# Optimization experiments

Hardware: AMD Instinct MI355X
Metric: run time of the kernel (lower is better)

Reference implementation:

```python
import jax, jax.numpy as jnp
import numpy as np

B, S, D, H = 4, 2048, 1024, 16
DEPTH = D // H


def setup_inputs() -> dict:
    key = jax.random.key(0)
    ks = jax.random.split(key, 12)
    inp = {
        "Q": jax.random.normal(ks[0], (B, S, D), jnp.float32),
        "K": jax.random.normal(ks[1], (B, S, D), jnp.float32),
        "V": jax.random.normal(ks[2], (B, S, D), jnp.float32),
        "mask": jax.random.randint(ks[3], (B, 1, S, S), 0, 2, jnp.int32),
        "Wq": jax.random.normal(ks[4], (D, D), jnp.float32) / np.sqrt(D),
        "bq": jnp.zeros((D,), jnp.float32),
        "Wk": jax.random.normal(ks[5], (D, D), jnp.float32) / np.sqrt(D),
        "bk": jnp.zeros((D,), jnp.float32),
        "Wv": jax.random.normal(ks[6], (D, D), jnp.float32) / np.sqrt(D),
        "bv": jnp.zeros((D,), jnp.float32),
        "Wo": jax.random.normal(ks[7], (D, D), jnp.float32) / np.sqrt(D),
        "bo": jnp.zeros((D,), jnp.float32),
    }
    return inp


def _split_heads(x):
    # (B, S, D) -> (B, H, S, depth)
    b, s, _ = x.shape
    return x.reshape(b, s, H, DEPTH).transpose(0, 2, 1, 3)


def reference(Q, K, V, mask, Wq, bq, Wk, bk, Wv, bv, Wo, bo):
    q = _split_heads(Q @ Wq + bq)  # (B,H,S,d)
    k = _split_heads(K @ Wk + bk)
    v = _split_heads(V @ Wv + bv)
    scores = jnp.einsum("bhqd,bhkd->bhqk", q, k) / jnp.sqrt(jnp.float32(DEPTH))
    m = mask.astype(jnp.bool_).astype(jnp.float32)  # (B,1,S,S)
    scores = scores + (1.0 - m) * -1e9
    attn = jax.nn.softmax(scores, axis=-1)  # (B,H,S,S)
    ctx = jnp.einsum("bhqk,bhkd->bhqd", attn, v)
    ctx = ctx.transpose(0, 2, 1, 3).reshape(Q.shape[0], -1, D)  # (B,S,D)
    out = ctx @ Wo + bo
    return out, attn
```

## Files before the change

kernel.cpp:

```cpp
#include <hip/hip_runtime.h>
#include <hip/hip_bf16.h>

#define B_ 4
#define S_ 2048
#define D_ 1024
#define H_ 16
#define TSZ 8388608L

typedef short short8 __attribute__((ext_vector_type(8)));
typedef float f32x4 __attribute__((ext_vector_type(4)));

__device__ inline unsigned short f2b(float f) {
  __hip_bfloat16 h = __float2bfloat16(f);
  return __builtin_bit_cast(unsigned short, h);
}
__device__ inline void gld16(const unsigned short* g, unsigned short* l) {
  __builtin_amdgcn_global_load_lds(
      (const __attribute__((address_space(1))) void*)g,
      (__attribute__((address_space(3))) void*)l, 16, 0, 0);
}

__global__ __launch_bounds__(256) void mask_pack(const int* __restrict__ mask,
                                                 unsigned int* __restrict__ mp) {
  long t = (long)blockIdx.x * 256 + threadIdx.x;
  const int4* p = (const int4*)(mask + (t >> 4) * (long)S_ + (t & 15) * 128);
  unsigned int w0 = 0, w1 = 0, w2 = 0, w3 = 0;
#pragma unroll
  for (int c = 0; c < 32; c++) {
    int4 v = p[c];
#pragma unroll
    for (int e = 0; e < 4; e++) {
      int k = c * 4 + e;
      int val = e == 0 ? v.x : e == 1 ? v.y : e == 2 ? v.z : v.w;
      int nb = k >> 4, p16 = k & 15;
      int gg = p16 >> 2, r = p16 & 3;
      unsigned bit = ((unsigned)val & 1u) << (nb * 4 + r);
      if (gg == 0) w0 |= bit; else if (gg == 1) w1 |= bit;
      else if (gg == 2) w2 |= bit; else w3 |= bit;
    }
  }
  *(uint4*)(mp + t * 4) = make_uint4(w0, w1, w2, w3);
}

__global__ __launch_bounds__(256) void cvt3(
    const float* __restrict__ Q, const float* __restrict__ K,
    const float* __restrict__ V, unsigned short* __restrict__ qo,
    unsigned short* __restrict__ ko, unsigned short* __restrict__ vo) {
  int seg = blockIdx.x >> 12;
  long i = ((long)(blockIdx.x & 4095) * 256 + threadIdx.x) * 8;
  const float* in = seg == 0 ? Q : seg == 1 ? K : V;
  unsigned short* out = seg == 0 ? qo : seg == 1 ? ko : vo;
  float4 a = *(const float4*)(in + i);
  float4 b = *(const float4*)(in + i + 4);
  short8 u;
  u[0] = (short)f2b(a.x); u[1] = (short)f2b(a.y);
  u[2] = (short)f2b(a.z); u[3] = (short)f2b(a.w);
  u[4] = (short)f2b(b.x); u[5] = (short)f2b(b.y);
  u[6] = (short)f2b(b.z); u[7] = (short)f2b(b.w);
  *(short8*)(out + i) = u;
}

__global__ __launch_bounds__(256) void transpose_w(
    const float* __restrict__ W, unsigned short* __restrict__ Wt) {
  __shared__ unsigned short t[64 * 72];
  const int tid = threadIdx.x;
  const int k0 = blockIdx.x * 64, n0 = blockIdx.y * 64;
#pragma unroll
  for (int p = 0; p < 4; p++) {
    int e = (p * 256 + tid) * 4;
    int r = e >> 6, c = e & 63;
    float4 v = *(const float4*)(W + (long)(k0 + r) * D_ + n0 + c);
    ushort4 u;
    u.x = f2b(v.x); u.y = f2b(v.y); u.z = f2b(v.z); u.w = f2b(v.w);
    *(ushort4*)(&t[r * 72 + c]) = u;
  }
  __syncthreads();
#pragma unroll
  for (int p = 0; p < 2; p++) {
    int e = (p * 256 + tid) * 8;
    int n = e >> 6, kc = e & 63;
    short8 x;
#pragma unroll
    for (int i = 0; i < 8; i++) x[i] = (short)t[(kc + i) * 72 + n];
    *(short8*)(Wt + (long)(n0 + n) * D_ + k0 + kc) = x;
  }
}

template <int MODE>
__global__ __launch_bounds__(256) void gemm_kernel(
    const unsigned short* __restrict__ A, const unsigned short* __restrict__ Wt,
    const float* __restrict__ bias, void* __restrict__ outv,
    int M, int N, int K) {
  __shared__ unsigned short Asm[128 * 32];
  __shared__ unsigned short Bsm[128 * 32];
  const int tid = threadIdx.x;
  const int lane = tid & 63, wid = tid >> 6;
  const int g = lane >> 4, li = lane & 15;
  const int wm = wid >> 1, wn = wid & 1;
  const long bm = (long)blockIdx.x * 128;
  const long bn = (long)blockIdx.y * 128;

  f32x4 acc[4][4];
#pragma unroll
  for (int i = 0; i < 4; i++)
#pragma unroll
    for (int j = 0; j < 4; j++) acc[i][j] = (f32x4){0.f, 0.f, 0.f, 0.f};

  for (int kt = 0; kt < K / 32; ++kt) {
    const int k0 = kt * 32;
    __syncthreads();
#pragma unroll
    for (int p = 0; p < 2; p++) {
      int ci = p * 256 + wid * 64 + lane;
      int r = ci >> 2, c = (ci & 3) * 8;
      gld16(A + (bm + r) * (long)K + k0 + c, &Asm[(p * 256 + wid * 64) * 8]);
      gld16(Wt + (bn + r) * (long)K + k0 + c, &Bsm[(p * 256 + wid * 64) * 8]);
    }
    __syncthreads();
    short8 af[4], bf[4];
#pragma unroll
    for (int i = 0; i < 4; i++)
      af[i] = *(const short8*)(&Asm[(wm * 64 + i * 16 + li) * 32 + g * 8]);
#pragma unroll
    for (int i = 0; i < 4; i++)
      bf[i] = *(const short8*)(&Bsm[(wn * 64 + i * 16 + li) * 32 + g * 8]);
#pragma unroll
    for (int i = 0; i < 4; i++)
#pragma unroll
      for (int j = 0; j < 4; j++)
        acc[i][j] =
            __builtin_amdgcn_mfma_f32_16x16x32_bf16(af[i], bf[j], acc[i][j], 0, 0, 0);
  }

#pragma unroll
  for (int i = 0; i < 4; i++) {
    int row0 = (int)bm + wm * 64 + i * 16 + g * 4;
#pragma unroll
    for (int j = 0; j < 4; j++) {
      int col = (int)bn + wn * 64 + j * 16 + li;
      float bvv = bias[col];
      if (MODE == 2) {
        int b = row0 >> 11, s0 = row0 & 2047;
        int h = col >> 6, dd = col & 63;
        ushort4 u;
#pragma unroll
        for (int jj = 0; jj < 4; jj++) u[jj] = f2b(acc[i][j][jj] + bvv);
        *(ushort4*)((unsigned short*)outv +
                    ((long)(b * H_ + h) * 64 + dd) * S_ + s0) = u;
      } else {
#pragma unroll
        for (int jj = 0; jj < 4; jj++) {
          int row = row0 + jj;
          float v = acc[i][j][jj] + bvv;
          if (MODE == 0) {
            ((float*)outv)[(long)row * N + col] = v;
          } else {
            int b = row >> 11, s = row & 2047;
            int h = col >> 6, dd = col & 63;
            ((unsigned short*)outv)[(((long)(b * H_ + h)) * S_ + s) * 64 + dd] =
                f2b(v);
          }
        }
      }
    }
  }
}

__global__ __launch_bounds__(256, 4) void attn_kernel(
    const unsigned short* __restrict__ q,
    const unsigned short* __restrict__ k,
    const unsigned short* __restrict__ vt,
    const unsigned int* __restrict__ mpk,
    float* __restrict__ attn,
    unsigned short* __restrict__ ctx) {
  __shared__ unsigned short k_lds[128 * 72];
  __shared__ unsigned short vt_lds[64 * 136];
  const int tid = threadIdx.x;
  const int lane = tid & 63, wid = tid >> 6;
  const int g = lane >> 4, li = lane & 15;
  const int bh = blockIdx.y;
  const int b = bh >> 4, h = bh & 15;
  const int qw = blockIdx.x * 64 + wid * 16;
  const int qs = qw + li;

  const unsigned short* qp = q + ((long)bh * S_ + qw) * 64;
  const short8 aq0 = *(const short8*)(qp + li * 64 + g * 8);
  const short8 aq1 = *(const short8*)(qp + li * 64 + 32 + g * 8);
  const unsigned int* mp = mpk + (((long)b * S_ + qs) * 16) * 4 + g;

  const unsigned short* kbase = k + (long)bh * S_ * 64;
  const unsigned short* vbase = vt + (long)bh * 64 * S_;
  int kst[4], kgo[4], vst[4], vgo[4];
#pragma unroll
  for (int p = 0; p < 4; p++) {
    int e = (p * 256 + tid) * 8;
    int krr = e >> 6, kcc = e & 63;
    kst[p] = krr * 72 + kcc;
    kgo[p] = krr * 64 + kcc;
    int vrr = e >> 7, vcc = e & 127;
    int c0 = ((vcc >> 5) << 5) + ((vcc & 8) << 1) + ((vcc & 16) >> 2);
    vst[p] = vrr * 136 + c0;
    vgo[p] = vrr * S_ + vcc;
  }

  float lsum = 0.f;
  short8 kreg[4];
#pragma unroll
  for (int p = 0; p < 4; p++)
    kreg[p] = *(const short8*)(kbase + kgo[p]);
  unsigned int mb_n = mp[0];
  for (int kt = 0; kt < 16; ++kt) {
    __syncthreads();
#pragma unroll
    for (int p = 0; p < 4; p++)
      *(short8*)(&k_lds[kst[p]]) = kreg[p];
    unsigned int mb = mb_n;
    if (kt < 15) {
#pragma unroll
      for (int p = 0; p < 4; p++)
        kreg[p] = *(const short8*)(kbase + (kt + 1) * 8192 + kgo[p]);
      mb_n = mp[(kt + 1) * 4];
    }
    __syncthreads();
#pragma unroll
    for (int nb = 0; nb < 8; nb++) {
      short8 b0 = *(const short8*)(&k_lds[(nb * 16 + li) * 72 + g * 8]);
      short8 b1 = *(const short8*)(&k_lds[(nb * 16 + li) * 72 + 32 + g * 8]);
      f32x4 s = (f32x4){0.f, 0.f, 0.f, 0.f};
      __builtin_amdgcn_s_setprio(1);
      s = __builtin_amdgcn_mfma_f32_16x16x32_bf16(b0, aq0, s, 0, 0, 0);
      s = __builtin_amdgcn_mfma_f32_16x16x32_bf16(b1, aq1, s, 0, 0, 0);
      __builtin_amdgcn_s_setprio(0);
#pragma unroll
      for (int r = 0; r < 4; r++) {
        float sc = s[r] * 0.125f + (((mb >> (nb * 4 + r)) & 1u) ? 0.f : -1e9f);
        lsum += __expf(sc);
      }
    }
  }
  lsum += __shfl_xor(lsum, 16);
  lsum += __shfl_xor(lsum, 32);
  const float linv = (lsum > 0.f) ? 1.0f / lsum : 0.f;

  f32x4 c[4];
#pragma unroll
  for (int i = 0; i < 4; i++) c[i] = (f32x4){0.f, 0.f, 0.f, 0.f};

  short8 vreg[4];
#pragma unroll
  for (int p = 0; p < 4; p++) {
    kreg[p] = *(const short8*)(kbase + kgo[p]);
    vreg[p] = *(const short8*)(vbase + vgo[p]);
  }
  mb_n = mp[0];
  for (int kt = 0; kt < 16; ++kt) {
    __syncthreads();
#pragma unroll
    for (int p = 0; p < 4; p++) {
      *(short8*)(&k_lds[kst[p]]) = kreg[p];
      ushort4* vh = (ushort4*)&vreg[p];
      *(ushort4*)(&vt_lds[vst[p]]) = vh[0];
      *(ushort4*)(&vt_lds[vst[p] + 8]) = vh[1];
    }
    unsigned int mb = mb_n;
    if (kt < 15) {
#pragma unroll
      for (int p = 0; p < 4; p++) {
        kreg[p] = *(const short8*)(kbase + (kt + 1) * 8192 + kgo[p]);
        vreg[p] = *(const short8*)(vbase + (kt + 1) * 128 + vgo[p]);
      }
      mb_n = mp[(kt + 1) * 4];
    }
    __syncthreads();
    float* arow = attn + ((long)bh * S_ + qs) * S_ + kt * 128;
    short8 pu2[4];
#pragma unroll
    for (int nb = 0; nb < 8; nb++) {
      short8 b0 = *(const short8*)(&k_lds[(nb * 16 + li) * 72 + g * 8]);
      short8 b1 = *(const short8*)(&k_lds[(nb * 16 + li) * 72 + 32 + g * 8]);
      f32x4 s = (f32x4){0.f, 0.f, 0.f, 0.f};
      __builtin_amdgcn_s_setprio(1);
      s = __builtin_amdgcn_mfma_f32_16x16x32_bf16(b0, aq0, s, 0, 0, 0);
      s = __builtin_amdgcn_mfma_f32_16x16x32_bf16(b1, aq1, s, 0, 0, 0);
      __builtin_amdgcn_s_setprio(0);
      f32x4 pf;
      ushort4 pu;
#pragma unroll
      for (int r = 0; r < 4; r++) {
        float sc = s[r] * 0.125f + (((mb >> (nb * 4 + r)) & 1u) ? 0.f : -1e9f);
        float pv = __expf(sc) * linv;
        pf[r] = pv;
        pu[r] = f2b(pv);
      }
      __builtin_nontemporal_store(pf, (f32x4*)(arow + nb * 16 + g * 4));
      ((ushort4*)&pu2[nb >> 1])[nb & 1] = pu;
    }
    __builtin_amdgcn_s_setprio(1);
#pragma unroll
    for (int kc = 0; kc < 4; kc++) {
      short8 ap = pu2[kc];
#pragma unroll
      for (int nb2 = 0; nb2 < 4; nb2++) {
        short8 bv =
            *(const short8*)(&vt_lds[(nb2 * 16 + li) * 136 + kc * 32 + g * 8]);
        c[nb2] = __builtin_amdgcn_mfma_f32_16x16x32_bf16(ap, bv, c[nb2], 0, 0, 0);
      }
    }
    __builtin_amdgcn_s_setprio(0);
  }

#pragma unroll
  for (int nb2 = 0; nb2 < 4; nb2++) {
#pragma unroll
    for (int j = 0; j < 4; j++) {
      int qrow = qw + g * 4 + j;
      ctx[((long)(b * S_ + qrow)) * D_ + h * 64 + nb2 * 16 + li] = f2b(c[nb2][j]);
    }
  }
}

extern "C" void kernel_launch(void* const* d_in, const int* in_sizes, int n_in,
                              void* d_out, int out_size, void* d_ws, size_t ws_size,
                              hipStream_t stream) {
  const float* Q = (const float*)d_in[0];
  const float* K = (const float*)d_in[1];
  const float* V = (const float*)d_in[2];
  const int* mask = (const int*)d_in[3];
  const float* Wq = (const float*)d_in[4];
  const float* bq = (const float*)d_in[5];
  const float* Wk = (const float*)d_in[6];
  const float* bk = (const float*)d_in[7];
  const float* Wv = (const float*)d_in[8];
  const float* bv = (const float*)d_in[9];
  const float* Wo = (const float*)d_in[10];
  const float* bo = (const float*)d_in[11];

  float* out = (float*)d_out;
  float* attn = out + TSZ;
  unsigned int* mpack = (unsigned int*)d_out;

  unsigned short* ws = (unsigned short*)d_ws;
  unsigned short* qh = ws;
  unsigned short* kh = ws + TSZ;
  unsigned short* vt = ws + 2 * TSZ;
  unsigned short* ctx = ws + 3 * TSZ;
  unsigned short* qbf = ws + 4 * TSZ;
  unsigned short* kbf = ws + 5 * TSZ;
  unsigned short* vbf = ws + 6 * TSZ;
  unsigned short* wtq = ws + 7 * TSZ;
  unsigned short* wtk = wtq + 1048576;
  unsigned short* wtv = wtk + 1048576;
  unsigned short* wto = wtv + 1048576;

  dim3 bb(256);
  mask_pack<<<512, bb, 0, stream>>>(mask, mpack);
  cvt3<<<12288, bb, 0, stream>>>(Q, K, V, qbf, kbf, vbf);
  transpose_w<<<dim3(16, 16), bb, 0, stream>>>(Wq, wtq);
  transpose_w<<<dim3(16, 16), bb, 0, stream>>>(Wk, wtk);
  transpose_w<<<dim3(16, 16), bb, 0, stream>>>(Wv, wtv);
  transpose_w<<<dim3(16, 16), bb, 0, stream>>>(Wo, wto);

  dim3 gg(64, 8);
  gemm_kernel<1><<<gg, bb, 0, stream>>>(qbf, wtq, bq, qh, 8192, 1024, 1024);
  gemm_kernel<1><<<gg, bb, 0, stream>>>(kbf, wtk, bk, kh, 8192, 1024, 1024);
  gemm_kernel<2><<<gg, bb, 0, stream>>>(vbf, wtv, bv, vt, 8192, 1024, 1024);
  attn_kernel<<<dim3(32, 64), bb, 0, stream>>>(qh, kh, vt, mpack, attn, ctx);
  gemm_kernel<0><<<gg, bb, 0, stream>>>(ctx, wto, bo, out, 8192, 1024, 1024);
}
```

Baseline: 559.7 us.

## Batch weight transposes and QKV GEMMs, read K directly from global in attention

Merges the four weight-transpose launches into one grid over z, and the three QKV projection GEMMs into one launch indexed by blockIdx.z. The Wo GEMM is specialised with constant sizes. In the attention kernel, K fragments are now loaded straight from global memory into registers, with no staging through LDS, which removes that LDS buffer and the barriers in the first pass. Blocks are also remapped so that each XCD handles a contiguous set of heads, for better L2 locality. The trade-off is more global or L2 traffic for K, with possible extra latency and less coalesced fragment loads, in exchange for less LDS use, fewer syncs and fewer launches.

```diff
diff --git a/kernel.cpp b/kernel.cpp
--- a/kernel.cpp
+++ b/kernel.cpp
@@ -60,9 +60,15 @@
   *(short8*)(out + i) = u;
 }
 
-__global__ __launch_bounds__(256) void transpose_w(
-    const float* __restrict__ W, unsigned short* __restrict__ Wt) {
+__global__ __launch_bounds__(256) void transpose_w4(
+    const float* __restrict__ W0, const float* __restrict__ W1,
+    const float* __restrict__ W2, const float* __restrict__ W3,
+    unsigned short* __restrict__ T0, unsigned short* __restrict__ T1,
+    unsigned short* __restrict__ T2, unsigned short* __restrict__ T3) {
   __shared__ unsigned short t[64 * 72];
+  const int z = blockIdx.z;
+  const float* W = z == 0 ? W0 : z == 1 ? W1 : z == 2 ? W2 : W3;
+  unsigned short* Wt = z == 0 ? T0 : z == 1 ? T1 : z == 2 ? T2 : T3;
   const int tid = threadIdx.x;
   const int k0 = blockIdx.x * 64, n0 = blockIdx.y * 64;
 #pragma unroll
@@ -86,11 +92,90 @@
   }
 }
 
-template <int MODE>
-__global__ __launch_bounds__(256) void gemm_kernel(
+__global__ __launch_bounds__(256) void qkv_gemm(
+    const unsigned short* __restrict__ qa, const unsigned short* __restrict__ ka,
+    const unsigned short* __restrict__ va, const unsigned short* __restrict__ wq,
+    const unsigned short* __restrict__ wk, const unsigned short* __restrict__ wv,
+    const float* __restrict__ bqp, const float* __restrict__ bkp,
+    const float* __restrict__ bvp, unsigned short* __restrict__ qo,
+    unsigned short* __restrict__ ko, unsigned short* __restrict__ vo) {
+  __shared__ unsigned short Asm[128 * 32];
+  __shared__ unsigned short Bsm[128 * 32];
+  const int z = blockIdx.z;
+  const unsigned short* A = z == 0 ? qa : z == 1 ? ka : va;
+  const unsigned short* Wt = z == 0 ? wq : z == 1 ? wk : wv;
+  const float* bias = z == 0 ? bqp : z == 1 ? bkp : bvp;
+  unsigned short* outp = z == 0 ? qo : z == 1 ? ko : vo;
+  const int tid = threadIdx.x;
+  const int lane = tid & 63, wid = tid >> 6;
+  const int g = lane >> 4, li = lane & 15;
+  const int wm = wid >> 1, wn = wid & 1;
+  const long bm = (long)blockIdx.x * 128;
+  const long bn = (long)blockIdx.y * 128;
+
+  f32x4 acc[4][4];
+#pragma unroll
+  for (int i = 0; i < 4; i++)
+#pragma unroll
+    for (int j = 0; j < 4; j++) acc[i][j] = (f32x4){0.f, 0.f, 0.f, 0.f};
+
+  for (int kt = 0; kt < 32; ++kt) {
+    const int k0 = kt * 32;
+    __syncthreads();
+#pragma unroll
+    for (int p = 0; p < 2; p++) {
+      int ci = p * 256 + wid * 64 + lane;
+      int r = ci >> 2, c = (ci & 3) * 8;
+      gld16(A + (bm + r) * 1024L + k0 + c, &Asm[(p * 256 + wid * 64) * 8]);
+      gld16(Wt + (bn + r) * 1024L + k0 + c, &Bsm[(p * 256 + wid * 64) * 8]);
+    }
+    __syncthreads();
+    short8 af[4], bf[4];
+#pragma unroll
+    for (int i = 0; i < 4; i++)
+      af[i] = *(const short8*)(&Asm[(wm * 64 + i * 16 + li) * 32 + g * 8]);
+#pragma unroll
+    for (int i = 0; i < 4; i++)
+      bf[i] = *(const short8*)(&Bsm[(wn * 64 + i * 16 + li) * 32 + g * 8]);
+#pragma unroll
+    for (int i = 0; i < 4; i++)
+#pragma unroll
+      for (int j = 0; j < 4; j++)
+        acc[i][j] =
+            __builtin_amdgcn_mfma_f32_16x16x32_bf16(af[i], bf[j], acc[i][j], 0, 0, 0);
+  }
+
+#pragma unroll
+  for (int i = 0; i < 4; i++) {
+    int row0 = (int)bm + wm * 64 + i * 16 + g * 4;
+#pragma unroll
+    for (int j = 0; j < 4; j++) {
+      int col = (int)bn + wn * 64 + j * 16 + li;
+      float bvv = bias[col];
+      if (z == 2) {
+        int b = row0 >> 11, s0 = row0 & 2047;
+        int h = col >> 6, dd = col & 63;
+        ushort4 u;
+#pragma unroll
+        for (int jj = 0; jj < 4; jj++) u[jj] = f2b(acc[i][j][jj] + bvv);
+        *(ushort4*)(outp + ((long)(b * H_ + h) * 64 + dd) * S_ + s0) = u;
+      } else {
+#pragma unroll
+        for (int jj = 0; jj < 4; jj++) {
+          int row = row0 + jj;
+          int b = row >> 11, s = row & 2047;
+          int h = col >> 6, dd = col & 63;
+          outp[(((long)(b * H_ + h)) * S_ + s) * 64 + dd] =
+              f2b(acc[i][j][jj] + bvv);
+        }
+      }
+    }
+  }
+}
+
+__global__ __launch_bounds__(256) void wo_gemm(
     const unsigned short* __restrict__ A, const unsigned short* __restrict__ Wt,
-    const float* __restrict__ bias, void* __restrict__ outv,
-    int M, int N, int K) {
+    const float* __restrict__ bias, float* __restrict__ out) {
   __shared__ unsigned short Asm[128 * 32];
   __shared__ unsigned short Bsm[128 * 32];
   const int tid = threadIdx.x;
@@ -106,15 +191,15 @@
 #pragma unroll
     for (int j = 0; j < 4; j++) acc[i][j] = (f32x4){0.f, 0.f, 0.f, 0.f};
 
-  for (int kt = 0; kt < K / 32; ++kt) {
+  for (int kt = 0; kt < 32; ++kt) {
     const int k0 = kt * 32;
     __syncthreads();
 #pragma unroll
     for (int p = 0; p < 2; p++) {
       int ci = p * 256 + wid * 64 + lane;
       int r = ci >> 2, c = (ci & 3) * 8;
-      gld16(A + (bm + r) * (long)K + k0 + c, &Asm[(p * 256 + wid * 64) * 8]);
-      gld16(Wt + (bn + r) * (long)K + k0 + c, &Bsm[(p * 256 + wid * 64) * 8]);
+      gld16(A + (bm + r) * 1024L + k0 + c, &Asm[(p * 256 + wid * 64) * 8]);
+      gld16(Wt + (bn + r) * 1024L + k0 + c, &Bsm[(p * 256 + wid * 64) * 8]);
     }
     __syncthreads();
     short8 af[4], bf[4];
@@ -139,29 +224,9 @@
     for (int j = 0; j < 4; j++) {
       int col = (int)bn + wn * 64 + j * 16 + li;
       float bvv = bias[col];
-      if (MODE == 2) {
-        int b = row0 >> 11, s0 = row0 & 2047;
-        int h = col >> 6, dd = col & 63;
-        ushort4 u;
-#pragma unroll
-        for (int jj = 0; jj < 4; jj++) u[jj] = f2b(acc[i][j][jj] + bvv);
-        *(ushort4*)((unsigned short*)outv +
-                    ((long)(b * H_ + h) * 64 + dd) * S_ + s0) = u;
-      } else {
-#pragma unroll
-        for (int jj = 0; jj < 4; jj++) {
-          int row = row0 + jj;
-          float v = acc[i][j][jj] + bvv;
-          if (MODE == 0) {
-            ((float*)outv)[(long)row * N + col] = v;
-          } else {
-            int b = row >> 11, s = row & 2047;
-            int h = col >> 6, dd = col & 63;
-            ((unsigned short*)outv)[(((long)(b * H_ + h)) * S_ + s) * 64 + dd] =
-                f2b(v);
-          }
-        }
-      }
+#pragma unroll
+      for (int jj = 0; jj < 4; jj++)
+        out[(long)(row0 + jj) * 1024 + col] = acc[i][j][jj] + bvv;
     }
   }
 }
@@ -173,14 +238,16 @@
     const unsigned int* __restrict__ mpk,
     float* __restrict__ attn,
     unsigned short* __restrict__ ctx) {
-  __shared__ unsigned short k_lds[128 * 72];
   __shared__ unsigned short vt_lds[64 * 136];
   const int tid = threadIdx.x;
   const int lane = tid & 63, wid = tid >> 6;
   const int g = lane >> 4, li = lane & 15;
-  const int bh = blockIdx.y;
+  const int p0 = blockIdx.x + 32 * blockIdx.y;
+  const int xcd = p0 & 7, q8 = p0 >> 3;
+  const int bx = q8 & 31;
+  const int bh = xcd * 8 + (q8 >> 5);
   const int b = bh >> 4, h = bh & 15;
-  const int qw = blockIdx.x * 64 + wid * 16;
+  const int qw = bx * 64 + wid * 16;
   const int qs = qw + li;
 
   const unsigned short* qp = q + ((long)bh * S_ + qw) * 64;
@@ -188,15 +255,12 @@
   const short8 aq1 = *(const short8*)(qp + li * 64 + 32 + g * 8);
   const unsigned int* mp = mpk + (((long)b * S_ + qs) * 16) * 4 + g;
 
-  const unsigned short* kbase = k + (long)bh * S_ * 64;
+  const unsigned short* kf = k + (long)bh * S_ * 64 + li * 64 + g * 8;
   const unsigned short* vbase = vt + (long)bh * 64 * S_;
-  int kst[4], kgo[4], vst[4], vgo[4];
+  int vst[4], vgo[4];
 #pragma unroll
   for (int p = 0; p < 4; p++) {
     int e = (p * 256 + tid) * 8;
-    int krr = e >> 6, kcc = e & 63;
-    kst[p] = krr * 72 + kcc;
-    kgo[p] = krr * 64 + kcc;
     int vrr = e >> 7, vcc = e & 127;
     int c0 = ((vcc >> 5) << 5) + ((vcc & 8) << 1) + ((vcc & 16) >> 2);
     vst[p] = vrr * 136 + c0;
@@ -204,37 +268,32 @@
   }
 
   float lsum = 0.f;
-  short8 kreg[4];
-#pragma unroll
-  for (int p = 0; p < 4; p++)
-    kreg[p] = *(const short8*)(kbase + kgo[p]);
   unsigned int mb_n = mp[0];
   for (int kt = 0; kt < 16; ++kt) {
-    __syncthreads();
-#pragma unroll
-    for (int p = 0; p < 4; p++)
-      *(short8*)(&k_lds[kst[p]]) = kreg[p];
     unsigned int mb = mb_n;
-    if (kt < 15) {
-#pragma unroll
-      for (int p = 0; p < 4; p++)
-        kreg[p] = *(const short8*)(kbase + (kt + 1) * 8192 + kgo[p]);
-      mb_n = mp[(kt + 1) * 4];
-    }
-    __syncthreads();
-#pragma unroll
-    for (int nb = 0; nb < 8; nb++) {
-      short8 b0 = *(const short8*)(&k_lds[(nb * 16 + li) * 72 + g * 8]);
-      short8 b1 = *(const short8*)(&k_lds[(nb * 16 + li) * 72 + 32 + g * 8]);
-      f32x4 s = (f32x4){0.f, 0.f, 0.f, 0.f};
-      __builtin_amdgcn_s_setprio(1);
-      s = __builtin_amdgcn_mfma_f32_16x16x32_bf16(b0, aq0, s, 0, 0, 0);
-      s = __builtin_amdgcn_mfma_f32_16x16x32_bf16(b1, aq1, s, 0, 0, 0);
-      __builtin_amdgcn_s_setprio(0);
-#pragma unroll
-      for (int r = 0; r < 4; r++) {
-        float sc = s[r] * 0.125f + (((mb >> (nb * 4 + r)) & 1u) ? 0.f : -1e9f);
-        lsum += __expf(sc);
+    if (kt < 15) mb_n = mp[(kt + 1) * 4];
+#pragma unroll
+    for (int nbh = 0; nbh < 2; ++nbh) {
+      short8 kb0[4], kb1[4];
+#pragma unroll
+      for (int i = 0; i < 4; i++) {
+        const unsigned short* kp2 = kf + (kt * 128 + (nbh * 4 + i) * 16) * 64;
+        kb0[i] = *(const short8*)(kp2);
+        kb1[i] = *(const short8*)(kp2 + 32);
+      }
+#pragma unroll
+      for (int i = 0; i < 4; i++) {
+        int nb = nbh * 4 + i;
+        f32x4 s = (f32x4){0.f, 0.f, 0.f, 0.f};
+        __builtin_amdgcn_s_setprio(1);
+        s = __builtin_amdgcn_mfma_f32_16x16x32_bf16(kb0[i], aq0, s, 0, 0, 0);
+        s = __builtin_amdgcn_mfma_f32_16x16x32_bf16(kb1[i], aq1, s, 0, 0, 0);
+        __builtin_amdgcn_s_setprio(0);
+#pragma unroll
+        for (int r = 0; r < 4; r++) {
+          float sc = s[r] * 0.125f + (((mb >> (nb * 4 + r)) & 1u) ? 0.f : -1e9f);
+          lsum += __expf(sc);
+        }
       }
     }
   }
@@ -248,16 +307,12 @@
 
   short8 vreg[4];
 #pragma unroll
-  for (int p = 0; p < 4; p++) {
-    kreg[p] = *(const short8*)(kbase + kgo[p]);
-    vreg[p] = *(const short8*)(vbase + vgo[p]);
-  }
+  for (int p = 0; p < 4; p++) vreg[p] = *(const short8*)(vbase + vgo[p]);
   mb_n = mp[0];
   for (int kt = 0; kt < 16; ++kt) {
     __syncthreads();
 #pragma unroll
     for (int p = 0; p < 4; p++) {
-      *(short8*)(&k_lds[kst[p]]) = kreg[p];
       ushort4* vh = (ushort4*)&vreg[p];
       *(ushort4*)(&vt_lds[vst[p]]) = vh[0];
       *(ushort4*)(&vt_lds[vst[p] + 8]) = vh[1];
@@ -265,35 +320,42 @@
     unsigned int mb = mb_n;
     if (kt < 15) {
 #pragma unroll
-      for (int p = 0; p < 4; p++) {
-        kreg[p] = *(const short8*)(kbase + (kt + 1) * 8192 + kgo[p]);
+      for (int p = 0; p < 4; p++)
         vreg[p] = *(const short8*)(vbase + (kt + 1) * 128 + vgo[p]);
-      }
       mb_n = mp[(kt + 1) * 4];
     }
     __syncthreads();
     float* arow = attn + ((long)bh * S_ + qs) * S_ + kt * 128;
     short8 pu2[4];
 #pragma unroll
-    for (int nb = 0; nb < 8; nb++) {
-      short8 b0 = *(const short8*)(&k_lds[(nb * 16 + li) * 72 + g * 8]);
-      short8 b1 = *(const short8*)(&k_lds[(nb * 16 + li) * 72 + 32 + g * 8]);
-      f32x4 s = (f32x4){0.f, 0.f, 0.f, 0.f};
-      __builtin_amdgcn_s_setprio(1);
-      s = __builtin_amdgcn_mfma_f32_16x16x32_bf16(b0, aq0, s, 0, 0, 0);
-      s = __builtin_amdgcn_mfma_f32_16x16x32_bf16(b1, aq1, s, 0, 0, 0);
-      __builtin_amdgcn_s_setprio(0);
-      f32x4 pf;
-      ushort4 pu;
-#pragma unroll
-      for (int r = 0; r < 4; r++) {
-        float sc = s[r] * 0.125f + (((mb >> (nb * 4 + r)) & 1u) ? 0.f : -1e9f);
-        float pv = __expf(sc) * linv;
-        pf[r] = pv;
-        pu[r] = f2b(pv);
-      }
-      __builtin_nontemporal_store(pf, (f32x4*)(arow + nb * 16 + g * 4));
-      ((ushort4*)&pu2[nb >> 1])[nb & 1] = pu;
+    for (int nbh = 0; nbh < 2; ++nbh) {
+      short8 kb0[4], kb1[4];
+#pragma unroll
+      for (int i = 0; i < 4; i++) {
+        const unsigned short* kp2 = kf + (kt * 128 + (nbh * 4 + i) * 16) * 64;
+        kb0[i] = *(const short8*)(kp2);
+        kb1[i] = *(const short8*)(kp2 + 32);
+      }
+#pragma unroll
+      for (int i = 0; i < 4; i++) {
+        int nb = nbh * 4 + i;
+        f32x4 s = (f32x4){0.f, 0.f, 0.f, 0.f};
+        __builtin_amdgcn_s_setprio(1);
+        s = __builtin_amdgcn_mfma_f32_16x16x32_bf16(kb0[i], aq0, s, 0, 0, 0);
+        s = __builtin_amdgcn_mfma_f32_16x16x32_bf16(kb1[i], aq1, s, 0, 0, 0);
+        __builtin_amdgcn_s_setprio(0);
+        f32x4 pf;
+        ushort4 pu;
+#pragma unroll
+        for (int r = 0; r < 4; r++) {
+          float sc = s[r] * 0.125f + (((mb >> (nb * 4 + r)) & 1u) ? 0.f : -1e9f);
+          float pv = __expf(sc) * linv;
+          pf[r] = pv;
+          pu[r] = f2b(pv);
+        }
+        __builtin_nontemporal_store(pf, (f32x4*)(arow + nb * 16 + g * 4));
+        ((ushort4*)&pu2[nb >> 1])[nb & 1] = pu;
+      }
     }
     __builtin_amdgcn_s_setprio(1);
 #pragma unroll
@@ -355,15 +417,10 @@
   dim3 bb(256);
   mask_pack<<<512, bb, 0, stream>>>(mask, mpack);
   cvt3<<<12288, bb, 0, stream>>>(Q, K, V, qbf, kbf, vbf);
-  transpose_w<<<dim3(16, 16), bb, 0, stream>>>(Wq, wtq);
-  transpose_w<<<dim3(16, 16), bb, 0, stream>>>(Wk, wtk);
-  transpose_w<<<dim3(16, 16), bb, 0, stream>>>(Wv, wtv);
-  transpose_w<<<dim3(16, 16), bb, 0, stream>>>(Wo, wto);
-
-  dim3 gg(64, 8);
-  gemm_kernel<1><<<gg, bb, 0, stream>>>(qbf, wtq, bq, qh, 8192, 1024, 1024);
-  gemm_kernel<1><<<gg, bb, 0, stream>>>(kbf, wtk, bk, kh, 8192, 1024, 1024);
-  gemm_kernel<2><<<gg, bb, 0, stream>>>(vbf, wtv, bv, vt, 8192, 1024, 1024);
+  transpose_w4<<<dim3(16, 16, 4), bb, 0, stream>>>(Wq, Wk, Wv, Wo, wtq, wtk,
+                                                   wtv, wto);
+  qkv_gemm<<<dim3(64, 8, 3), bb, 0, stream>>>(qbf, kbf, vbf, wtq, wtk, wtv, bq,
+                                              bk, bv, qh, kh, vt);
   attn_kernel<<<dim3(32, 64), bb, 0, stream>>>(qh, kh, vt, mpack, attn, ctx);
-  gemm_kernel<0><<<gg, bb, 0, stream>>>(ctx, wto, bo, out, 8192, 1024, 1024);
-}
+  wo_gemm<<<dim3(64, 8), bb, 0, stream>>>(ctx, wto, bo, out);
+}
```

After: 676.4 us. +20.9%, slower.
